# Performance work log

Hardware: AMD Instinct MI355X
Metric: run time of the kernel (lower is better)

Reference implementation:

```python
import jax, jax.numpy as jnp
import numpy as np
import math

D_MODEL = 1024
N_HEADS = 16
HEAD_DIM = D_MODEL // N_HEADS


def rotate_half(x):
    x1, x2 = x[..., : x.shape[-1] // 2], x[..., x.shape[-1] // 2 :]
    return jnp.concatenate([-x2, x1], axis=-1)


def rope_cos_sin(T, dim, dtype):
    inv_freq = 1.0 / (10000.0 ** (jnp.arange(0, dim, 2, dtype=jnp.float32) / dim))
    t = jnp.arange(T, dtype=jnp.float32)
    freqs = jnp.einsum('i,j->ij', t, inv_freq)          # [T, dim/2]
    emb = jnp.concatenate([freqs, freqs], axis=-1)      # [T, dim]
    # broadcast shape [1, T, 1, dim] to match q/k of shape [B, T, H, dim]
    return emb.astype(dtype)[None, :, None, :]


def setup_inputs() -> dict:
    key = jax.random.key(0)
    k_x, k_qkv_w, k_qkv_b, k_p_w, k_p_b = jax.random.split(key, 5)
    B, T = 2, 2048
    s = 1.0 / math.sqrt(D_MODEL)
    return {
        'x': jax.random.normal(k_x, (B, T, D_MODEL), dtype=jnp.float32),
        'qkv_w': jax.random.uniform(k_qkv_w, (3 * D_MODEL, D_MODEL), minval=-s, maxval=s, dtype=jnp.float32),
        'qkv_b': jax.random.uniform(k_qkv_b, (3 * D_MODEL,), minval=-s, maxval=s, dtype=jnp.float32),
        'proj_w': jax.random.uniform(k_p_w, (D_MODEL, D_MODEL), minval=-s, maxval=s, dtype=jnp.float32),
        'proj_b': jax.random.uniform(k_p_b, (D_MODEL,), minval=-s, maxval=s, dtype=jnp.float32),
    }


def reference(x, qkv_w, qkv_b, proj_w, proj_b):
    B, T, C = x.shape
    H, Dh = N_HEADS, HEAD_DIM
    qkv = x @ qkv_w.T + qkv_b                           # [B, T, 3C]
    qkv = qkv.reshape(B, T, 3, H, Dh)
    q, k, v = qkv[:, :, 0], qkv[:, :, 1], qkv[:, :, 2]  # [B, T, H, Dh]
    emb = rope_cos_sin(T, Dh, x.dtype)
    cos, sin = jnp.cos(emb), jnp.sin(emb)
    q = q * cos + rotate_half(q) * sin
    k = k * cos + rotate_half(k) * sin
    # attention with causal mask (dropout in eval mode = identity)
    scale = 1.0 / math.sqrt(Dh)
    attn = jnp.einsum('bqhd,bkhd->bhqk', q, k) * scale  # [B, H, T, T]
    causal = jnp.tril(jnp.ones((T, T), dtype=bool))
    attn = jnp.where(causal, attn, -jnp.inf)
    attn = jax.nn.softmax(attn, axis=-1)
    out = jnp.einsum('bhqk,bkhd->bqhd', attn, v).reshape(B, T, C)
    return out @ proj_w.T + proj_b
```

## Files before the change

kernel.cpp:

```cpp
#include <hip/hip_runtime.h>
#include <math.h>

#define T_SEQ 2048
#define NB 2
#define NH 16
#define DH 64
#define DM 1024

typedef unsigned short u16;
typedef __attribute__((ext_vector_type(8))) __bf16 bf16x8;
typedef __attribute__((ext_vector_type(4))) __bf16 bf16v4;
typedef __attribute__((ext_vector_type(4))) short s16x4;
typedef __attribute__((ext_vector_type(4))) float f32x4;
typedef __attribute__((ext_vector_type(4))) int i32x4;

__device__ __forceinline__ u16 f2bf(float f) {
  return __builtin_bit_cast(u16, (__bf16)f);
}
__device__ __forceinline__ float bf2f(u16 v) {
  unsigned u = ((unsigned)v) << 16;
  return __builtin_bit_cast(float, u);
}
__device__ __forceinline__ bf16x8 ld_frag(const u16* p) {
  bf16x8 r; __builtin_memcpy(&r, p, 16); return r;
}
__device__ __forceinline__ s16x4 ld8(const u16* p) {
  s16x4 r; __builtin_memcpy(&r, p, 8); return r;
}
__device__ __forceinline__ i32x4 ld16(const u16* p) {
  i32x4 r; __builtin_memcpy(&r, p, 16); return r;
}
__device__ __forceinline__ void st16(u16* p, i32x4 v) {
  __builtin_memcpy(p, &v, 16);
}
__device__ __forceinline__ void cvt_store8(u16* dst, const float* src) {
  f32x4 a, b;
  __builtin_memcpy(&a, src, 16);
  __builtin_memcpy(&b, src + 4, 16);
  bf16x8 t;
  t[0] = (__bf16)a[0]; t[1] = (__bf16)a[1]; t[2] = (__bf16)a[2]; t[3] = (__bf16)a[3];
  t[4] = (__bf16)b[0]; t[5] = (__bf16)b[1]; t[6] = (__bf16)b[2]; t[7] = (__bf16)b[3];
  __builtin_memcpy(dst, &t, 16);
}
__device__ __forceinline__ void gld_lds16(const u16* g, u16* l) {
  __builtin_amdgcn_global_load_lds(
      (const __attribute__((address_space(1))) void*)g,
      (__attribute__((address_space(3))) void*)l, 16, 0, 0);
}

__global__ __launch_bounds__(256) void cvt_f32_bf16(const float* __restrict__ in,
                                                    u16* __restrict__ out, int n8) {
  const int i = blockIdx.x * 256 + threadIdx.x;
  if (i < n8) cvt_store8(out + (long)i * 8, in + (long)i * 8);
}

__global__ __launch_bounds__(256) void cvt2_f32_bf16(
    const float* __restrict__ inA, u16* __restrict__ outA, int n8A,
    const float* __restrict__ inB, u16* __restrict__ outB, int n8B,
    int blocksA) {
  if ((int)blockIdx.x < blocksA) {
    const int i = blockIdx.x * 256 + threadIdx.x;
    if (i < n8A) cvt_store8(outA + (long)i * 8, inA + (long)i * 8);
  } else {
    const int i = (blockIdx.x - blocksA) * 256 + threadIdx.x;
    if (i < n8B) cvt_store8(outB + (long)i * 8, inB + (long)i * 8);
  }
}

template <int MODE, int BN>
__global__ __launch_bounds__(256) void gemm_nt(
    const u16* __restrict__ A, const u16* __restrict__ Bw,
    const float* __restrict__ bias, float* __restrict__ out,
    u16* __restrict__ q_ws, u16* __restrict__ k_ws, u16* __restrict__ v_ws,
    int M, int N, int K) {
  constexpr int NTN = BN / 32;
  constexpr int WNS = BN / 2;
  __shared__ __align__(16) u16 As[128 * 32];
  __shared__ __align__(16) u16 Bs[BN * 32];
  const int tid = threadIdx.x;
  const int wave = tid >> 6, lane = tid & 63;
  const int quad = lane >> 4, l16 = lane & 15;
  const int wm = wave & 1, wn = wave >> 1;
  const int m0 = blockIdx.y * 128, n0 = blockIdx.x * BN;
  const int lrow = lane >> 2;
  const int lcol = (lane & 3) * 8;

  f32x4 acc[4][NTN] = {};

  const u16* Ag = A + (long)(m0 + wave * 16 + lrow) * K + lcol;
  const u16* Bg = Bw + (long)(n0 + wave * 16 + lrow) * K + lcol;
  u16* Al = &As[(wave * 16 + lrow) * 32 + lcol];
  u16* Bl = &Bs[(wave * 16 + lrow) * 32 + lcol];

  for (int k0 = 0; k0 < K; k0 += 32) {
    __syncthreads();
    gld_lds16(Ag + k0, Al);
    gld_lds16(Ag + (long)64 * K + k0, Al + 64 * 32);
    gld_lds16(Bg + k0, Bl);
    if constexpr (BN == 128) gld_lds16(Bg + (long)64 * K + k0, Bl + 64 * 32);
    __syncthreads();
    bf16x8 af[4], bfr[NTN];
#pragma unroll
    for (int mt = 0; mt < 4; mt++)
      af[mt] = ld_frag(&As[(wm * 64 + mt * 16 + l16) * 32 + quad * 8]);
#pragma unroll
    for (int nt = 0; nt < NTN; nt++)
      bfr[nt] = ld_frag(&Bs[(wn * WNS + nt * 16 + l16) * 32 + quad * 8]);
#pragma unroll
    for (int mt = 0; mt < 4; mt++)
#pragma unroll
      for (int nt = 0; nt < NTN; nt++)
        acc[mt][nt] = __builtin_amdgcn_mfma_f32_16x16x32_bf16(af[mt], bfr[nt],
                                                              acc[mt][nt], 0, 0, 0);
  }

  if constexpr (MODE == 1) {
#pragma unroll
    for (int nt = 0; nt < NTN; nt++) {
      const int col = n0 + wn * WNS + nt * 16 + l16;
      const float bv = bias[col];
#pragma unroll
      for (int mt = 0; mt < 4; mt++) {
        const int rbase = m0 + wm * 64 + mt * 16 + quad * 4;
#pragma unroll
        for (int r = 0; r < 4; r++)
          out[(long)(rbase + r) * N + col] = acc[mt][nt][r] + bv;
      }
    }
  } else {
    const int which = n0 >> 10;
#pragma unroll
    for (int np = 0; np < 2; np++) {
      const int col1 = n0 + wn * 64 + np * 16 + l16;
      const int rem = col1 & 1023;
      const int h = rem >> 6, dh = rem & 63;
      const float bv1 = bias[col1], bv2 = bias[col1 + 32];
      if (which == 2) {
#pragma unroll
        for (int mt = 0; mt < 4; mt++) {
          const int rbase = m0 + wm * 64 + mt * 16 + quad * 4;
          const int b = rbase >> 11;
#pragma unroll
          for (int r = 0; r < 4; r++) {
            const int t = (rbase + r) & (T_SEQ - 1);
            const long vb = (((long)(b * NH + h)) * DH) * T_SEQ + t;
            v_ws[vb + (long)dh * T_SEQ] = f2bf(acc[mt][np][r] + bv1);
            v_ws[vb + (long)(dh + 32) * T_SEQ] = f2bf(acc[mt][np + 2][r] + bv2);
          }
        }
      } else {
        const float invf = exp2f(-(float)dh * 0.41524101186092045f);
        const float cD = cosf(invf), sD = sinf(invf);
        u16* dst = (which == 0) ? q_ws : k_ws;
        const float sc = (which == 0) ? 0.125f : 1.0f;
#pragma unroll
        for (int mt = 0; mt < 4; mt++) {
          const int rbase = m0 + wm * 64 + mt * 16 + quad * 4;
          const int b = rbase >> 11;
          const int t0 = rbase & (T_SEQ - 1);
          float c = cosf((float)t0 * invf), s = sinf((float)t0 * invf);
#pragma unroll
          for (int r = 0; r < 4; r++) {
            const float v1 = acc[mt][np][r] + bv1;
            const float v2 = acc[mt][np + 2][r] + bv2;
            const float o1 = (v1 * c - v2 * s) * sc;
            const float o2 = (v2 * c + v1 * s) * sc;
            const long ib = (((long)(b * NH + h)) * T_SEQ + (t0 + r)) * DH;
            dst[ib + dh] = f2bf(o1);
            dst[ib + dh + 32] = f2bf(o2);
            const float cn = c * cD - s * sD;
            s = s * cD + c * sD;
            c = cn;
          }
        }
      }
    }
  }
}

__global__ __launch_bounds__(256, 4) void attn_kernel(const u16* __restrict__ q,
                                                      const u16* __restrict__ k,
                                                      const u16* __restrict__ v,
                                                      u16* __restrict__ o) {
  __shared__ __align__(16) u16 Ks[128 * 72];
  __shared__ __align__(16) u16 Vt[64 * 136];
  const int tid = threadIdx.x;
  const int wave = tid >> 6, lane = tid & 63;
  const int quad = lane >> 4, l16 = lane & 15;
  const int bh = blockIdx.x;
  const int y = blockIdx.y;
  const int kk = y >> 3, a = y & 7;
  const int qt = (kk == 0) ? (2 * a)
               : (kk == 1) ? (31 - 2 * a)
               : (kk == 2) ? (2 * a + 1)
                           : (30 - 2 * a);
  const long base = (long)bh * T_SEQ * DH;
  const int b = bh >> 4, h = bh & 15;

  const int q0 = qt * 64;
  const int qrow = q0 + wave * 16 + l16;
  bf16x8 bq0, bq1;
  {
    const u16* qr = q + base + (long)qrow * DH + quad * 8;
    bq0 = ld_frag(qr);
    bq1 = ld_frag(qr + 32);
  }
  float lst = 0.f;
  f32x4 oacc[4] = {};
  const int nkt = (q0 + 64 + 127) >> 7;

  const int k_rr = tid >> 3;
  const int k_cc = (tid & 7) * 8;
  const int v_d  = tid >> 4;
  const int v_cc = (tid & 15) * 8;
  const u16* kbase = k + base;
  const u16* vbase = v + base;

  i32x4 kreg[4], vreg[4];
#pragma unroll
  for (int p = 0; p < 4; p++) {
    kreg[p] = ld16(kbase + (long)(k_rr + p * 32) * DH + k_cc);
    vreg[p] = ld16(vbase + (long)(v_d + p * 16) * T_SEQ + v_cc);
  }
#pragma unroll
  for (int p = 0; p < 4; p++) {
    st16(&Ks[(k_rr + p * 32) * 72 + k_cc], kreg[p]);
    st16(&Vt[(v_d + p * 16) * 136 + v_cc], vreg[p]);
  }
  __syncthreads();

  for (int kt = 0; kt < nkt; kt++) {
    const int key0 = kt * 128;
    const bool last = (kt == nkt - 1);

    if (!last) {
      const int kn = key0 + 128;
#pragma unroll
      for (int p = 0; p < 4; p++) {
        kreg[p] = ld16(kbase + (long)kn * DH + (long)(k_rr + p * 32) * DH + k_cc);
        vreg[p] = ld16(vbase + kn + (long)(v_d + p * 16) * T_SEQ + v_cc);
      }
    }

#pragma unroll
    for (int hh = 0; hh < 2; hh++) {
      if (hh == 1 && last && key0 >= q0) continue;
      const int kb = key0 + hh * 64;

      f32x4 sfr[4];
      __builtin_amdgcn_s_setprio(1);
#pragma unroll
      for (int nt = 0; nt < 4; nt++) {
        const int row = hh * 64 + nt * 16 + l16;
        bf16x8 k0f = ld_frag(&Ks[row * 72 + quad * 8]);
        bf16x8 k1f = ld_frag(&Ks[row * 72 + 32 + quad * 8]);
        f32x4 z = {0.f, 0.f, 0.f, 0.f};
        z = __builtin_amdgcn_mfma_f32_16x16x32_bf16(k0f, bq0, z, 0, 0, 0);
        z = __builtin_amdgcn_mfma_f32_16x16x32_bf16(k1f, bq1, z, 0, 0, 0);
        sfr[nt] = z;
      }
      __builtin_amdgcn_s_setprio(0);

      if (last) {
#pragma unroll
        for (int nt = 0; nt < 4; nt++) {
          const int keyb = kb + nt * 16 + quad * 4;
#pragma unroll
          for (int r = 0; r < 4; r++)
            sfr[nt][r] = (keyb + r <= qrow) ? sfr[nt][r] : -1e30f;
        }
      }

      float rsum = 0.f;
      s16x4 pf[4];
#pragma unroll
      for (int nt = 0; nt < 4; nt++) {
        bf16v4 pv;
#pragma unroll
        for (int r = 0; r < 4; r++) {
          const float p =
              exp2f(__builtin_fmaf(sfr[nt][r], 1.44269504f, -46.166241f));
          rsum += p;
          pv[r] = (__bf16)p;
        }
        pf[nt] = __builtin_bit_cast(s16x4, pv);
      }
      rsum += __shfl_xor(rsum, 16, 64);
      rsum += __shfl_xor(rsum, 32, 64);
      lst += rsum;

      __builtin_amdgcn_s_setprio(1);
#pragma unroll
      for (int ont = 0; ont < 4; ont++) {
        const u16* vrow = &Vt[(ont * 16 + l16) * 136 + hh * 64 + quad * 4];
#pragma unroll
        for (int nt = 0; nt < 4; nt++) {
          s16x4 vf = ld8(vrow + nt * 16);
          oacc[ont] = __builtin_amdgcn_mfma_f32_16x16x16bf16_1k(vf, pf[nt],
                                                                oacc[ont], 0, 0, 0);
        }
      }
      __builtin_amdgcn_s_setprio(0);
    }

    if (!last) {
      __syncthreads();
#pragma unroll
      for (int p = 0; p < 4; p++) {
        st16(&Ks[(k_rr + p * 32) * 72 + k_cc], kreg[p]);
        st16(&Vt[(v_d + p * 16) * 136 + v_cc], vreg[p]);
      }
      __syncthreads();
    }
  }

  const float inv_l = 1.f / lst;
  u16* orow = o + ((long)(b * T_SEQ + qrow)) * DM + h * DH + quad * 4;
#pragma unroll
  for (int ont = 0; ont < 4; ont++) {
    bf16v4 t4;
#pragma unroll
    for (int r = 0; r < 4; r++) t4[r] = (__bf16)(oacc[ont][r] * inv_l);
    __builtin_memcpy(orow + ont * 16, &t4, 8);
  }
}

extern "C" void kernel_launch(void* const* d_in, const int* in_sizes, int n_in,
                              void* d_out, int out_size, void* d_ws, size_t ws_size,
                              hipStream_t stream) {
  const float* x      = (const float*)d_in[0];
  const float* qkv_w  = (const float*)d_in[1];
  const float* qkv_b  = (const float*)d_in[2];
  const float* proj_w = (const float*)d_in[3];
  const float* proj_b = (const float*)d_in[4];
  float* out = (float*)d_out;

  u16* ws = (u16*)d_ws;
  const long per = (long)NB * NH * T_SEQ * DH;
  u16* q_ws = ws;
  u16* k_ws = ws + per;
  u16* v_ws = ws + 2 * per;
  u16* ao_ws = ws + 3 * per;
  u16* x_bf  = ws + 3 * per;
  u16* w_bf  = ws + 4 * per;

  dim3 blk(256);
  cvt2_f32_bf16<<<2048 + 1536, blk, 0, stream>>>(
      x, x_bf, (int)(per / 8), qkv_w, w_bf, 3 * DM * DM / 8, 2048);
  gemm_nt<0, 128><<<dim3(24, 32), blk, 0, stream>>>(x_bf, w_bf, qkv_b, nullptr,
                                                    q_ws, k_ws, v_ws, 4096, 3072, 1024);
  attn_kernel<<<dim3(32, 32), blk, 0, stream>>>(q_ws, k_ws, v_ws, ao_ws);
  cvt_f32_bf16<<<512, blk, 0, stream>>>(proj_w, w_bf, DM * DM / 8);
  gemm_nt<1, 64><<<dim3(16, 32), blk, 0, stream>>>(ao_ws, w_bf, proj_b, out,
                                                   nullptr, nullptr, nullptr, 4096, 1024, 1024);
}
```

Baseline: 190.9 us.

## Split attention key range across two wave groups and merge partial outputs

The attention kernel now launches 512 threads per block: two groups of four waves each handle the same 64 query rows but process disjoint halves of the causal key blocks, using 64-key tiles and separate shared-memory buffers. At the end, group 1 writes its partial accumulators and row sums to shared memory and group 0 adds them before normalising and storing. This roughly halves the serial key loop per block to cut latency for long causal rows. The cost is extra block-wide barriers, a shared-memory reduction step, and launch bounds of 8 that may squeeze registers.

```diff
diff --git a/kernel.cpp b/kernel.cpp
--- a/kernel.cpp
+++ b/kernel.cpp
@@ -178,14 +178,15 @@
   }
 }
 
-__global__ __launch_bounds__(256, 4) void attn_kernel(const u16* __restrict__ q,
+__global__ __launch_bounds__(512, 8) void attn_kernel(const u16* __restrict__ q,
                                                       const u16* __restrict__ k,
                                                       const u16* __restrict__ v,
                                                       u16* __restrict__ o) {
-  __shared__ __align__(16) u16 Ks[128 * 72];
-  __shared__ __align__(16) u16 Vt[64 * 136];
+  __shared__ __align__(16) u16 sm[2 * 9216];
   const int tid = threadIdx.x;
   const int wave = tid >> 6, lane = tid & 63;
+  const int grp = wave >> 2;
+  const int w4 = wave & 3;
   const int quad = lane >> 4, l16 = lane & 15;
   const int bh = blockIdx.x;
   const int y = blockIdx.y;
@@ -198,7 +199,7 @@
   const int b = bh >> 4, h = bh & 15;
 
   const int q0 = qt * 64;
-  const int qrow = q0 + wave * 16 + l16;
+  const int qrow = q0 + w4 * 16 + l16;
   bf16x8 bq0, bq1;
   {
     const u16* qr = q + base + (long)qrow * DH + quad * 8;
@@ -207,51 +208,58 @@
   }
   float lst = 0.f;
   f32x4 oacc[4] = {};
-  const int nkt = (q0 + 64 + 127) >> 7;
-
-  const int k_rr = tid >> 3;
-  const int k_cc = (tid & 7) * 8;
-  const int v_d  = tid >> 4;
-  const int v_cc = (tid & 15) * 8;
+
+  const int nTot = qt + 1;
+  const int nA = nTot >> 1;
+  const int nB = nTot - nA;
+  const int sb0 = grp ? nA : 0;
+  const int nG = grp ? nB : nA;
+
+  u16* Ks = sm + grp * 9216;
+  u16* Vt = sm + grp * 9216 + 4608;
+
+  const int tg = tid & 255;
+  const int s_rr = tg >> 3;
+  const int s_cc = (tg & 7) * 8;
   const u16* kbase = k + base;
   const u16* vbase = v + base;
 
-  i32x4 kreg[4], vreg[4];
-#pragma unroll
-  for (int p = 0; p < 4; p++) {
-    kreg[p] = ld16(kbase + (long)(k_rr + p * 32) * DH + k_cc);
-    vreg[p] = ld16(vbase + (long)(v_d + p * 16) * T_SEQ + v_cc);
-  }
-#pragma unroll
-  for (int p = 0; p < 4; p++) {
-    st16(&Ks[(k_rr + p * 32) * 72 + k_cc], kreg[p]);
-    st16(&Vt[(v_d + p * 16) * 136 + v_cc], vreg[p]);
+  i32x4 kreg[2], vreg[2];
+  if (nG > 0) {
+    const int kb = sb0 * 64;
+#pragma unroll
+    for (int p = 0; p < 2; p++) {
+      kreg[p] = ld16(kbase + (long)(kb + s_rr + p * 32) * DH + s_cc);
+      vreg[p] = ld16(vbase + kb + (long)(s_rr + p * 32) * T_SEQ + s_cc);
+    }
+#pragma unroll
+    for (int p = 0; p < 2; p++) {
+      st16(&Ks[(s_rr + p * 32) * 72 + s_cc], kreg[p]);
+      st16(&Vt[(s_rr + p * 32) * 72 + s_cc], vreg[p]);
+    }
   }
   __syncthreads();
 
-  for (int kt = 0; kt < nkt; kt++) {
-    const int key0 = kt * 128;
-    const bool last = (kt == nkt - 1);
-
-    if (!last) {
-      const int kn = key0 + 128;
-#pragma unroll
-      for (int p = 0; p < 4; p++) {
-        kreg[p] = ld16(kbase + (long)kn * DH + (long)(k_rr + p * 32) * DH + k_cc);
-        vreg[p] = ld16(vbase + kn + (long)(v_d + p * 16) * T_SEQ + v_cc);
-      }
-    }
-
-#pragma unroll
-    for (int hh = 0; hh < 2; hh++) {
-      if (hh == 1 && last && key0 >= q0) continue;
-      const int kb = key0 + hh * 64;
-
+  for (int it = 0; it < nB; it++) {
+    const bool act = it < nG;
+    const int sb = sb0 + it;
+
+    if (it + 1 < nG) {
+      const int kn = (sb + 1) * 64;
+#pragma unroll
+      for (int p = 0; p < 2; p++) {
+        kreg[p] = ld16(kbase + (long)(kn + s_rr + p * 32) * DH + s_cc);
+        vreg[p] = ld16(vbase + kn + (long)(s_rr + p * 32) * T_SEQ + s_cc);
+      }
+    }
+
+    if (act) {
+      const int kb = sb * 64;
       f32x4 sfr[4];
       __builtin_amdgcn_s_setprio(1);
 #pragma unroll
       for (int nt = 0; nt < 4; nt++) {
-        const int row = hh * 64 + nt * 16 + l16;
+        const int row = nt * 16 + l16;
         bf16x8 k0f = ld_frag(&Ks[row * 72 + quad * 8]);
         bf16x8 k1f = ld_frag(&Ks[row * 72 + 32 + quad * 8]);
         f32x4 z = {0.f, 0.f, 0.f, 0.f};
@@ -261,7 +269,7 @@
       }
       __builtin_amdgcn_s_setprio(0);
 
-      if (last) {
+      if (grp == 1 && it == nB - 1) {
 #pragma unroll
         for (int nt = 0; nt < 4; nt++) {
           const int keyb = kb + nt * 16 + quad * 4;
@@ -292,7 +300,7 @@
       __builtin_amdgcn_s_setprio(1);
 #pragma unroll
       for (int ont = 0; ont < 4; ont++) {
-        const u16* vrow = &Vt[(ont * 16 + l16) * 136 + hh * 64 + quad * 4];
+        const u16* vrow = &Vt[(ont * 16 + l16) * 72 + quad * 4];
 #pragma unroll
         for (int nt = 0; nt < 4; nt++) {
           s16x4 vf = ld8(vrow + nt * 16);
@@ -303,25 +311,45 @@
       __builtin_amdgcn_s_setprio(0);
     }
 
-    if (!last) {
-      __syncthreads();
-#pragma unroll
-      for (int p = 0; p < 4; p++) {
-        st16(&Ks[(k_rr + p * 32) * 72 + k_cc], kreg[p]);
-        st16(&Vt[(v_d + p * 16) * 136 + v_cc], vreg[p]);
-      }
-      __syncthreads();
-    }
-  }
-
-  const float inv_l = 1.f / lst;
-  u16* orow = o + ((long)(b * T_SEQ + qrow)) * DM + h * DH + quad * 4;
-#pragma unroll
-  for (int ont = 0; ont < 4; ont++) {
-    bf16v4 t4;
-#pragma unroll
-    for (int r = 0; r < 4; r++) t4[r] = (__bf16)(oacc[ont][r] * inv_l);
-    __builtin_memcpy(orow + ont * 16, &t4, 8);
+    __syncthreads();
+    if (it + 1 < nG) {
+#pragma unroll
+      for (int p = 0; p < 2; p++) {
+        st16(&Ks[(s_rr + p * 32) * 72 + s_cc], kreg[p]);
+        st16(&Vt[(s_rr + p * 32) * 72 + s_cc], vreg[p]);
+      }
+    }
+    __syncthreads();
+  }
+
+  float* cmb = (float*)sm;
+  float* lsb = cmb + 4 * 16 * 65;
+  if (grp == 1) {
+#pragma unroll
+    for (int ont = 0; ont < 4; ont++)
+#pragma unroll
+      for (int r = 0; r < 4; r++)
+        cmb[(w4 * 16 + l16) * 65 + ont * 16 + quad * 4 + r] = oacc[ont][r];
+    if (quad == 0) lsb[w4 * 16 + l16] = lst;
+  }
+  __syncthreads();
+  if (grp == 0) {
+#pragma unroll
+    for (int ont = 0; ont < 4; ont++)
+#pragma unroll
+      for (int r = 0; r < 4; r++)
+        oacc[ont][r] += cmb[(w4 * 16 + l16) * 65 + ont * 16 + quad * 4 + r];
+    lst += lsb[w4 * 16 + l16];
+
+    const float inv_l = 1.f / lst;
+    u16* orow = o + ((long)(b * T_SEQ + qrow)) * DM + h * DH + quad * 4;
+#pragma unroll
+    for (int ont = 0; ont < 4; ont++) {
+      bf16v4 t4;
+#pragma unroll
+      for (int r = 0; r < 4; r++) t4[r] = (__bf16)(oacc[ont][r] * inv_l);
+      __builtin_memcpy(orow + ont * 16, &t4, 8);
+    }
   }
 }
 
@@ -349,7 +377,7 @@
       x, x_bf, (int)(per / 8), qkv_w, w_bf, 3 * DM * DM / 8, 2048);
   gemm_nt<0, 128><<<dim3(24, 32), blk, 0, stream>>>(x_bf, w_bf, qkv_b, nullptr,
                                                     q_ws, k_ws, v_ws, 4096, 3072, 1024);
-  attn_kernel<<<dim3(32, 32), blk, 0, stream>>>(q_ws, k_ws, v_ws, ao_ws);
+  attn_kernel<<<dim3(32, 32), dim3(512), 0, stream>>>(q_ws, k_ws, v_ws, ao_ws);
   cvt_f32_bf16<<<512, blk, 0, stream>>>(proj_w, w_bf, DM * DM / 8);
   gemm_nt<1, 64><<<dim3(16, 32), blk, 0, stream>>>(ao_ws, w_bf, proj_b, out,
                                                    nullptr, nullptr, nullptr, 4096, 1024, 1024);
```

New measurement: 258.0 us. +35.1%, slower.

## Split long causal query tiles across two KV halves with combine kernel

Applied to the files above, without the earlier changes.

Query tiles in the upper half of the sequence are processed by two blocks, each covering half of the key range. They write unnormalized fp32 partial outputs and row sums to workspace, and a new combine kernel sums them and normalizes. The aim is more parallelism and less per-block imbalance in the causal attention kernel. The cost is an extra launch and fp32 partial-output traffic, and the path only runs when the workspace is large enough.

```diff
diff --git a/kernel.cpp b/kernel.cpp
--- a/kernel.cpp
+++ b/kernel.cpp
@@ -178,10 +178,13 @@
   }
 }
 
+template <int SPLIT>
 __global__ __launch_bounds__(256, 4) void attn_kernel(const u16* __restrict__ q,
                                                       const u16* __restrict__ k,
                                                       const u16* __restrict__ v,
-                                                      u16* __restrict__ o) {
+                                                      u16* __restrict__ o,
+                                                      float* __restrict__ po,
+                                                      float* __restrict__ pl) {
   __shared__ __align__(16) u16 Ks[128 * 72];
   __shared__ __align__(16) u16 Vt[64 * 136];
   const int tid = threadIdx.x;
@@ -189,15 +192,30 @@
   const int quad = lane >> 4, l16 = lane & 15;
   const int bh = blockIdx.x;
   const int y = blockIdx.y;
-  const int kk = y >> 3, a = y & 7;
-  const int qt = (kk == 0) ? (2 * a)
-               : (kk == 1) ? (31 - 2 * a)
-               : (kk == 2) ? (2 * a + 1)
-                           : (30 - 2 * a);
+
+  int qt, piece;
+  if constexpr (SPLIT == 0) {
+    const int kk = y >> 3, a = y & 7;
+    qt = (kk == 0) ? (2 * a)
+       : (kk == 1) ? (31 - 2 * a)
+       : (kk == 2) ? (2 * a + 1)
+                   : (30 - 2 * a);
+    piece = -1;
+  } else {
+    if (y < 16)      { qt = y;      piece = -1; }
+    else if (y < 32) { qt = y;      piece = 0;  }
+    else             { qt = y - 16; piece = 1;  }
+  }
+  const int q0 = qt * 64;
+  const int nkt = (q0 + 64 + 127) >> 7;
+  const int nf = nkt >> 1;
+  const int kt0 = (piece == 1) ? nf : 0;
+  const int ktN = (piece == 0) ? nf : nkt;
+  const bool hasDiag = (piece != 0);
+
   const long base = (long)bh * T_SEQ * DH;
   const int b = bh >> 4, h = bh & 15;
 
-  const int q0 = qt * 64;
   const int qrow = q0 + wave * 16 + l16;
   bf16x8 bq0, bq1;
   {
@@ -207,7 +225,6 @@
   }
   float lst = 0.f;
   f32x4 oacc[4] = {};
-  const int nkt = (q0 + 64 + 127) >> 7;
 
   const int k_rr = tid >> 3;
   const int k_cc = (tid & 7) * 8;
@@ -217,34 +234,37 @@
   const u16* vbase = v + base;
 
   i32x4 kreg[4], vreg[4];
-#pragma unroll
-  for (int p = 0; p < 4; p++) {
-    kreg[p] = ld16(kbase + (long)(k_rr + p * 32) * DH + k_cc);
-    vreg[p] = ld16(vbase + (long)(v_d + p * 16) * T_SEQ + v_cc);
-  }
-#pragma unroll
-  for (int p = 0; p < 4; p++) {
-    st16(&Ks[(k_rr + p * 32) * 72 + k_cc], kreg[p]);
-    st16(&Vt[(v_d + p * 16) * 136 + v_cc], vreg[p]);
+  {
+    const int kbeg = kt0 * 128;
+#pragma unroll
+    for (int p = 0; p < 4; p++) {
+      kreg[p] = ld16(kbase + (long)(kbeg + k_rr + p * 32) * DH + k_cc);
+      vreg[p] = ld16(vbase + kbeg + (long)(v_d + p * 16) * T_SEQ + v_cc);
+    }
+#pragma unroll
+    for (int p = 0; p < 4; p++) {
+      st16(&Ks[(k_rr + p * 32) * 72 + k_cc], kreg[p]);
+      st16(&Vt[(v_d + p * 16) * 136 + v_cc], vreg[p]);
+    }
   }
   __syncthreads();
 
-  for (int kt = 0; kt < nkt; kt++) {
+  for (int kt = kt0; kt < ktN; kt++) {
     const int key0 = kt * 128;
-    const bool last = (kt == nkt - 1);
-
-    if (!last) {
+    const bool dlast = hasDiag && (kt == ktN - 1);
+
+    if (kt + 1 < ktN) {
       const int kn = key0 + 128;
 #pragma unroll
       for (int p = 0; p < 4; p++) {
-        kreg[p] = ld16(kbase + (long)kn * DH + (long)(k_rr + p * 32) * DH + k_cc);
+        kreg[p] = ld16(kbase + (long)(kn + k_rr + p * 32) * DH + k_cc);
         vreg[p] = ld16(vbase + kn + (long)(v_d + p * 16) * T_SEQ + v_cc);
       }
     }
 
 #pragma unroll
     for (int hh = 0; hh < 2; hh++) {
-      if (hh == 1 && last && key0 >= q0) continue;
+      if (hh == 1 && dlast && key0 >= q0) continue;
       const int kb = key0 + hh * 64;
 
       f32x4 sfr[4];
@@ -261,7 +281,7 @@
       }
       __builtin_amdgcn_s_setprio(0);
 
-      if (last) {
+      if (dlast) {
 #pragma unroll
         for (int nt = 0; nt < 4; nt++) {
           const int keyb = kb + nt * 16 + quad * 4;
@@ -303,7 +323,7 @@
       __builtin_amdgcn_s_setprio(0);
     }
 
-    if (!last) {
+    if (kt + 1 < ktN) {
       __syncthreads();
 #pragma unroll
       for (int p = 0; p < 4; p++) {
@@ -314,15 +334,50 @@
     }
   }
 
-  const float inv_l = 1.f / lst;
-  u16* orow = o + ((long)(b * T_SEQ + qrow)) * DM + h * DH + quad * 4;
-#pragma unroll
-  for (int ont = 0; ont < 4; ont++) {
-    bf16v4 t4;
-#pragma unroll
-    for (int r = 0; r < 4; r++) t4[r] = (__bf16)(oacc[ont][r] * inv_l);
-    __builtin_memcpy(orow + ont * 16, &t4, 8);
-  }
+  if (SPLIT == 0 || piece < 0) {
+    const float inv_l = 1.f / lst;
+    u16* orow = o + ((long)(b * T_SEQ + qrow)) * DM + h * DH + quad * 4;
+#pragma unroll
+    for (int ont = 0; ont < 4; ont++) {
+      bf16v4 t4;
+#pragma unroll
+      for (int r = 0; r < 4; r++) t4[r] = (__bf16)(oacc[ont][r] * inv_l);
+      __builtin_memcpy(orow + ont * 16, &t4, 8);
+    }
+  } else {
+    const long idx = (long)(bh * 16 + (qt - 16)) * 2 + piece;
+    float* pob = po + idx * 4096;
+#pragma unroll
+    for (int ont = 0; ont < 4; ont++) {
+      f32x4 vv = oacc[ont];
+      __builtin_memcpy(&pob[(wave * 16 + l16) * 64 + ont * 16 + quad * 4], &vv, 16);
+    }
+    if (quad == 0) pl[idx * 64 + wave * 16 + l16] = lst;
+  }
+}
+
+__global__ __launch_bounds__(256) void attn_combine(const float* __restrict__ po,
+                                                    const float* __restrict__ pl,
+                                                    u16* __restrict__ o) {
+  const int bh = blockIdx.x, j = blockIdx.y;
+  const int qt = 16 + j, b = bh >> 4, h = bh & 15, q0 = qt * 64;
+  const int t = threadIdx.x, qq = t >> 2, dg = t & 3;
+  const long ia = ((long)(bh * 16 + j) * 2) * 4096;
+  const long ib = ia + 4096;
+  const float lsum = pl[((long)(bh * 16 + j) * 2) * 64 + qq] +
+                     pl[((long)(bh * 16 + j) * 2 + 1) * 64 + qq];
+  const float inv_l = 1.f / lsum;
+  u16 outb[16];
+#pragma unroll
+  for (int k2 = 0; k2 < 4; k2++) {
+    f32x4 aa, bb;
+    __builtin_memcpy(&aa, &po[ia + qq * 64 + dg * 16 + k2 * 4], 16);
+    __builtin_memcpy(&bb, &po[ib + qq * 64 + dg * 16 + k2 * 4], 16);
+#pragma unroll
+    for (int r = 0; r < 4; r++) outb[k2 * 4 + r] = f2bf((aa[r] + bb[r]) * inv_l);
+  }
+  u16* orow = o + ((long)(b * T_SEQ + q0 + qq)) * DM + h * DH + dg * 16;
+  __builtin_memcpy(orow, outb, 32);
 }
 
 extern "C" void kernel_launch(void* const* d_in, const int* in_sizes, int n_in,
@@ -343,13 +398,22 @@
   u16* ao_ws = ws + 3 * per;
   u16* x_bf  = ws + 3 * per;
   u16* w_bf  = ws + 4 * per;
+  const size_t base_bytes = (size_t)(4 * per + 3 * DM * DM) * 2;
+  float* po = (float*)((char*)d_ws + base_bytes);
+  float* pl = po + (long)32 * 16 * 2 * 4096;
+  const size_t need = base_bytes + (size_t)(32 * 16 * 2) * (4096 + 64) * 4;
 
   dim3 blk(256);
   cvt2_f32_bf16<<<2048 + 1536, blk, 0, stream>>>(
       x, x_bf, (int)(per / 8), qkv_w, w_bf, 3 * DM * DM / 8, 2048);
   gemm_nt<0, 128><<<dim3(24, 32), blk, 0, stream>>>(x_bf, w_bf, qkv_b, nullptr,
                                                     q_ws, k_ws, v_ws, 4096, 3072, 1024);
-  attn_kernel<<<dim3(32, 32), blk, 0, stream>>>(q_ws, k_ws, v_ws, ao_ws);
+  if (ws_size >= need) {
+    attn_kernel<1><<<dim3(32, 48), blk, 0, stream>>>(q_ws, k_ws, v_ws, ao_ws, po, pl);
+    attn_combine<<<dim3(32, 16), blk, 0, stream>>>(po, pl, ao_ws);
+  } else {
+    attn_kernel<0><<<dim3(32, 32), blk, 0, stream>>>(q_ws, k_ws, v_ws, ao_ws, po, pl);
+  }
   cvt_f32_bf16<<<512, blk, 0, stream>>>(proj_w, w_bf, DM * DM / 8);
   gemm_nt<1, 64><<<dim3(16, 32), blk, 0, stream>>>(ao_ws, w_bf, proj_b, out,
                                                    nullptr, nullptr, nullptr, 4096, 1024, 1024);
```

Result: slower. 197.4 us (+3.4%).
